# Performance work log

Measured on AMD Instinct MI355X. Metric: run time of the kernel, lower is better.

Reference implementation:

```python
import jax, jax.numpy as jnp
import numpy as np

IN_C = 256
CC = 256
K_HP = 3  # highpass_kernel
ENC_K = 3  # encoder_kernel, dilation 1 -> padding 1


def _conv2d(x, w, b, pad):
    # x: [n, ci, h, w], w: [co, ci, kh, kw] (OIHW), b: [co]
    y = jax.lax.conv_general_dilated(
        x, w, window_strides=(1, 1), padding=((pad, pad), (pad, pad)),
        dimension_numbers=("NCHW", "OIHW", "NCHW"))
    return y + b[None, :, None, None]


def _kernel_normalizer(mask, k, hamming_flat):
    # mask: [n, k*k, h, w] (mask_channel = 1, scale_factor = 1 -> pixel_shuffle is identity)
    n, kc, h, w = mask.shape
    m = jax.nn.softmax(mask, axis=1)              # softmax over the k*k kernel taps
    m = m * hamming_flat[None, :, None, None]     # per-tap hamming window (row-major kxk)
    m = m / jnp.sum(m, axis=1, keepdims=True)     # renormalize to sum 1 per pixel
    return m


def _carafe(x, mask, k):
    # Content-aware reassembly, scale=1, group=1.
    # out[n,c,h,w] = sum_{i,j} mask[n, i*k+j, h, w] * x[n, c, h+i-k//2, w+j-k//2]
    pad = k // 2
    n, c, h, w = x.shape
    xp = jnp.pad(x, ((0, 0), (0, 0), (pad, pad), (pad, pad)))
    out = jnp.zeros_like(x)
    for i in range(k):
        for j in range(k):
            out = out + mask[:, i * k + j][:, None] * xp[:, :, i:i + h, j:j + w]
    return out


def setup_inputs() -> dict:
    key = jax.random.key(0)
    ks = jax.random.split(key, 6)
    n, h, w = 4, 128, 128
    s = 0.02
    x = jax.random.normal(ks[0], (n, IN_C, h, w), jnp.float32)
    w_comp = jax.random.normal(ks[1], (CC, IN_C, 1, 1), jnp.float32) * s
    b_comp = jnp.zeros((CC,), jnp.float32)
    w_hp = jax.random.normal(ks[2], (K_HP * K_HP, CC, ENC_K, ENC_K), jnp.float32) * s
    b_hp = jnp.zeros((K_HP * K_HP,), jnp.float32)
    w_res = jax.random.normal(ks[3], (CC, CC, ENC_K, ENC_K), jnp.float32) * s
    b_res = jnp.zeros((CC,), jnp.float32)
    w_mul = jax.random.normal(ks[4], (CC, CC, ENC_K, ENC_K), jnp.float32) * s
    b_mul = jnp.zeros((CC,), jnp.float32)
    ham = np.outer(np.hamming(K_HP), np.hamming(K_HP)).astype(np.float32).reshape(-1)
    hamming_hp = jnp.asarray(ham)
    return {"x": x, "w_comp": w_comp, "b_comp": b_comp, "w_hp": w_hp, "b_hp": b_hp,
            "w_res": w_res, "b_res": b_res, "w_mul": w_mul, "b_mul": b_mul,
            "hamming_hp": hamming_hp}


def reference(x, w_comp, b_comp, w_hp, b_hp, w_res, b_res, w_mul, b_mul, hamming_hp):
    compressed = _conv2d(x, w_comp, b_comp, 0)
    # high-pass branch: dynamic-kernel generation + CARAFE reassembly
    filt = _conv2d(compressed, w_hp, b_hp, (ENC_K - 1) // 2)
    filt = _kernel_normalizer(filt, K_HP, hamming_hp)
    feat_hp = x - _carafe(x, filt, K_HP)
    # additive residual branch
    feat_add = x + _conv2d(compressed, w_res, b_res, (ENC_K - 1) // 2)
    # multiplicative gating branch
    feat_mul = x * _conv2d(compressed, w_mul, b_mul, (ENC_K - 1) // 2)
    return (feat_hp, feat_add, feat_mul)
```

## Files before the change

### kernel.cpp

```cpp
#include <hip/hip_runtime.h>
#include <hip/hip_bf16.h>

#define NIMG 4
#define C    256
#define H    128
#define W    128
#define HW   (H*W)
#define CHW  (C*HW)
#define TOT  (NIMG*CHW)

typedef short bf16x8 __attribute__((ext_vector_type(8)));
typedef unsigned short ushort8 __attribute__((ext_vector_type(8)));
typedef float f32x16 __attribute__((ext_vector_type(16)));
typedef unsigned short u16;

__device__ inline u16 f2bf(float f) {
    __hip_bfloat16 h = __float2bfloat16(f);
    return __builtin_bit_cast(u16, h);
}

__device__ __forceinline__ int swzB(int byte) {
    return byte ^ (((byte >> 7) & 1) << 4) ^ (((byte >> 8) & 3) << 5);
}

__global__ __launch_bounds__(256)
void prep_w_kernel(const float* __restrict__ w_hp, const float* __restrict__ w_res,
                   const float* __restrict__ w_mul, const float* __restrict__ w_comp,
                   u16* __restrict__ wcat, u16* __restrict__ wbf)
{
    int i = blockIdx.x * 256 + threadIdx.x;
    const int NW = 576 * 2304;
    if (i < NW) {
        int co = i / 2304, r = i - co * 2304;
        int tap = r >> 8, ci = r & 255;
        float v = 0.f;
        if (co < 9)        v = w_hp[co * 2304 + ci * 9 + tap];
        else if (co < 265) v = w_res[(co - 9) * 2304 + ci * 9 + tap];
        else if (co < 521) v = w_mul[(co - 265) * 2304 + ci * 9 + tap];
        wcat[i] = f2bf(v);
    } else if (i < NW + 65536) {
        int j = i - NW;
        wbf[j] = f2bf(w_comp[j]);
    }
}

__global__ __launch_bounds__(256)
void conv1x1_mfma_kernel(const float* __restrict__ x, const u16* __restrict__ wbf,
                         const float* __restrict__ b, u16* __restrict__ comp)
{
    __shared__ u16 As[64 * 40];
    __shared__ u16 Bs[256 * 40];

    const int pt  = blockIdx.x;
    const int n   = pt >> 6;
    const int hw0 = (pt & 63) * 256;
    const int co0 = blockIdx.y * 64;

    const int tid  = threadIdx.x;
    const int wv   = tid >> 6;
    const int lane = tid & 63;
    const int l31  = lane & 31;
    const int lh   = lane >> 5;

    f32x16 acc[2][2];
    #pragma unroll
    for (int cf = 0; cf < 2; ++cf)
        #pragma unroll
        for (int p = 0; p < 2; ++p)
            #pragma unroll
            for (int e = 0; e < 16; ++e) acc[cf][p][e] = 0.f;

    for (int c0 = 0; c0 < 256; c0 += 32) {
        #pragma unroll
        for (int r = 0; r < 2; ++r) {
            int l  = tid + 256*r;
            int co = l >> 3, cq = l & 7;
            ushort4 v = *(const ushort4*)(wbf + (co0+co)*256 + c0 + cq*4);
            *(ushort4*)(As + co*40 + cq*4) = v;
        }
        #pragma unroll
        for (int r = 0; r < 2; ++r) {
            int l = tid + 256*r;
            int q = l & 7, g = l >> 3;
            const float* src = x + (long)n*CHW + (long)(c0 + q*4)*HW + hw0 + g*4;
            float4 v0 = *(const float4*)(src);
            float4 v1 = *(const float4*)(src + HW);
            float4 v2 = *(const float4*)(src + 2*HW);
            float4 v3 = *(const float4*)(src + 3*HW);
            u16* dst = Bs + (g*4)*40 + q*4;
            *(ushort4*)(dst)       = make_ushort4(f2bf(v0.x), f2bf(v1.x), f2bf(v2.x), f2bf(v3.x));
            *(ushort4*)(dst + 40)  = make_ushort4(f2bf(v0.y), f2bf(v1.y), f2bf(v2.y), f2bf(v3.y));
            *(ushort4*)(dst + 80)  = make_ushort4(f2bf(v0.z), f2bf(v1.z), f2bf(v2.z), f2bf(v3.z));
            *(ushort4*)(dst + 120) = make_ushort4(f2bf(v0.w), f2bf(v1.w), f2bf(v2.w), f2bf(v3.w));
        }
        __syncthreads();
        #pragma unroll
        for (int kk = 0; kk < 2; ++kk) {
            bf16x8 a0 = *(const bf16x8*)(As + (l31     )*40 + kk*16 + lh*8);
            bf16x8 a1 = *(const bf16x8*)(As + (l31 + 32)*40 + kk*16 + lh*8);
            #pragma unroll
            for (int p = 0; p < 2; ++p) {
                bf16x8 bb = *(const bf16x8*)(Bs + (wv*64 + p*32 + l31)*40 + kk*16 + lh*8);
                acc[0][p] = __builtin_amdgcn_mfma_f32_32x32x16_bf16(a0, bb, acc[0][p], 0, 0, 0);
                acc[1][p] = __builtin_amdgcn_mfma_f32_32x32x16_bf16(a1, bb, acc[1][p], 0, 0, 0);
            }
        }
        __syncthreads();
    }

    #pragma unroll
    for (int cf = 0; cf < 2; ++cf) {
        #pragma unroll
        for (int p = 0; p < 2; ++p) {
            int pos = hw0 + wv*64 + p*32 + l31;
            #pragma unroll
            for (int reg = 0; reg < 16; ++reg) {
                int row = (reg & 3) + 8*(reg >> 2) + 4*lh;
                int co  = co0 + cf*32 + row;
                comp[(long)n*CHW + (long)co*HW + pos] = f2bf(acc[cf][p][reg] + b[co]);
            }
        }
    }
}

__global__ __launch_bounds__(256, 3)
void conv3x3_mfma_kernel(const u16* __restrict__ comp, const u16* __restrict__ wcat,
                         const float* __restrict__ xin,
                         const float* __restrict__ b_hp, const float* __restrict__ b_res,
                         const float* __restrict__ b_mul,
                         float* __restrict__ out, float* __restrict__ filt_raw)
{
    __shared__ u16 As[64 * 152];
    __shared__ u16 Bs[4 * 132 * 16];

    const int id  = blockIdx.x + 256 * blockIdx.y;
    const int xcd = id & 7;
    const int rr_ = id >> 3;
    const int ct  = rr_ % 9;
    const int pt  = (xcd << 5) + rr_ / 9;

    const int n   = pt >> 6;
    const int y0  = (pt & 63) * 2;
    const int co0 = ct * 64;

    const int tid  = threadIdx.x;
    const int wv   = tid >> 6;
    const int lane = tid & 63;
    const int l31  = lane & 31;
    const int lh   = lane >> 5;
    const int row  = wv & 1;
    const int ch   = wv >> 1;

    for (int i = tid; i < 4*132*16/2; i += 256) ((int*)Bs)[i] = 0;

    f32x16 acc[2][2];
    #pragma unroll
    for (int cf = 0; cf < 2; ++cf)
        #pragma unroll
        for (int p = 0; p < 2; ++p)
            #pragma unroll
            for (int e = 0; e < 16; ++e) acc[cf][p][e] = 0.f;

    const u16* wbase = wcat + (long)co0 * 2304;

    const u16* asrc[5]; u16* adst[5]; bool avld[5];
    #pragma unroll
    for (int r = 0; r < 5; ++r) {
        int l = tid + 256*r;
        avld[r] = (l < 1152);
        int ll = avld[r] ? l : 0;
        int co = ll / 18, s = ll - co*18;
        asrc[r] = wbase + co*2304 + (s >> 1)*256 + (s & 1)*8;
        adst[r] = As + co*152 + s*8;
    }

    const int bh  = lh;
    const int bcg = l31;
    const int byy = y0 - 1 + wv;
    const bool bv = (byy >= 0 && byy < H);
    const u16* bsrc = comp + ((long)n*C + bh*8)*HW + (bv ? byy : 0)*W + bcg*4;

    __syncthreads();

    ushort8 pa[5];
    #pragma unroll
    for (int r = 0; r < 5; ++r)
        if (avld[r]) pa[r] = *(const ushort8*)(asrc[r]);
    ushort4 pb[8];
    if (bv) {
        #pragma unroll
        for (int j = 0; j < 8; ++j) pb[j] = *(const ushort4*)(bsrc + (long)j*HW);
    }

    for (int c = 0; c < 16; ++c) {
        #pragma unroll
        for (int r = 0; r < 5; ++r)
            if (avld[r]) *(ushort8*)(adst[r]) = pa[r];
        if (bv) {
            #pragma unroll
            for (int cw = 0; cw < 4; ++cw) {
                ushort8 v;
                #pragma unroll
                for (int j = 0; j < 8; ++j) v[j] = ((const u16*)&pb[j])[cw];
                int byteoff = ((wv*132 + bcg*4 + 1 + cw) << 5) + (bh << 4);
                *(ushort8*)((char*)Bs + swzB(byteoff)) = v;
            }
        }
        __syncthreads();
        if (c < 15) {
            const int c0n = (c + 1) * 16;
            #pragma unroll
            for (int r = 0; r < 5; ++r)
                if (avld[r]) pa[r] = *(const ushort8*)(asrc[r] + c0n);
            if (bv) {
                const u16* s = bsrc + (long)c0n*HW;
                #pragma unroll
                for (int j = 0; j < 8; ++j) pb[j] = *(const ushort4*)(s + (long)j*HW);
            }
        }
        #pragma unroll
        for (int tap = 0; tap < 9; ++tap) {
            const int kh = tap / 3, kw = tap - kh*3;
            bf16x8 a0 = *(const bf16x8*)((const char*)As + l31*304      + tap*32 + lh*16);
            bf16x8 a1 = *(const bf16x8*)((const char*)As + (l31+32)*304 + tap*32 + lh*16);
            #pragma unroll
            for (int p = 0; p < 2; ++p) {
                int byteoff = (((row + kh)*132 + ch*64 + p*32 + l31 + kw) << 5) + (lh << 4);
                bf16x8 bb = *(const bf16x8*)((const char*)Bs + swzB(byteoff));
                acc[0][p] = __builtin_amdgcn_mfma_f32_32x32x16_bf16(a0, bb, acc[0][p], 0, 0, 0);
                acc[1][p] = __builtin_amdgcn_mfma_f32_32x32x16_bf16(a1, bb, acc[1][p], 0, 0, 0);
            }
        }
        __syncthreads();
    }

    const int yrow = y0 + row;
    #pragma unroll
    for (int cf = 0; cf < 2; ++cf) {
        #pragma unroll
        for (int p = 0; p < 2; ++p) {
            int xx = ch*64 + p*32 + l31;
            #pragma unroll
            for (int reg = 0; reg < 16; ++reg) {
                int rw = (reg & 3) + 8*(reg >> 2) + 4*lh;
                int co = co0 + cf*32 + rw;
                float v = acc[cf][p][reg];
                if (co < 9) {
                    filt_raw[((long)n*9 + co)*HW + yrow*W + xx] = v + b_hp[co];
                } else if (co < 265) {
                    int cc = co - 9;
                    long idx = (long)n*CHW + (long)cc*HW + yrow*W + xx;
                    out[(long)TOT + idx] = xin[idx] + v + b_res[cc];
                } else if (co < 521) {
                    int cc = co - 265;
                    long idx = (long)n*CHW + (long)cc*HW + yrow*W + xx;
                    out[2L*TOT + idx] = xin[idx] * (v + b_mul[cc]);
                }
            }
        }
    }
}

__global__ __launch_bounds__(256)
void carafe_hp_kernel(const float* __restrict__ x, const float* __restrict__ filt_raw,
                      const float* __restrict__ ham, float* __restrict__ out)
{
    const int id = blockIdx.x;
    const int pt = ((id & 7) << 6) + (id >> 3);
    const int n  = pt >> 7;
    const int y  = pt & 127;
    const int pg = threadIdx.x & 31;
    const int cs = threadIdx.x >> 5;
    const int x0 = pg * 4;

    float4 wt[9];
    {
        const float* fr = filt_raw + (long)n*9*HW + y*W + x0;
        #pragma unroll
        for (int t = 0; t < 9; ++t) wt[t] = *(const float4*)(fr + t*HW);
        float4 mx = wt[0];
        #pragma unroll
        for (int t = 1; t < 9; ++t) {
            mx.x = fmaxf(mx.x, wt[t].x); mx.y = fmaxf(mx.y, wt[t].y);
            mx.z = fmaxf(mx.z, wt[t].z); mx.w = fmaxf(mx.w, wt[t].w);
        }
        float4 s = make_float4(0,0,0,0);
        #pragma unroll
        for (int t = 0; t < 9; ++t) {
            float hm = ham[t];
            wt[t].x = expf(wt[t].x - mx.x) * hm; s.x += wt[t].x;
            wt[t].y = expf(wt[t].y - mx.y) * hm; s.y += wt[t].y;
            wt[t].z = expf(wt[t].z - mx.z) * hm; s.z += wt[t].z;
            wt[t].w = expf(wt[t].w - mx.w) * hm; s.w += wt[t].w;
        }
        float4 inv = make_float4(1.f/s.x, 1.f/s.y, 1.f/s.z, 1.f/s.w);
        #pragma unroll
        for (int t = 0; t < 9; ++t) {
            wt[t].x *= inv.x; wt[t].y *= inv.y; wt[t].z *= inv.z; wt[t].w *= inv.w;
        }
    }

    const float* xb = x   + (long)n*CHW + (long)y*W + x0;
    float*       ob = out + (long)n*CHW + (long)y*W + x0;

    for (int i = 0; i < 32; ++i) {
        int c = cs*32 + i;
        const float* xc = xb + (long)c*HW;
        float rr[3][6];
        #pragma unroll
        for (int dh = 0; dh < 3; ++dh) {
            int yy = y - 1 + dh;
            if (yy >= 0 && yy < H) {
                const float* p = xc + (dh-1)*W;
                float4 v = *(const float4*)p;
                rr[dh][0] = (x0 > 0)     ? p[-1] : 0.f;
                rr[dh][1] = v.x; rr[dh][2] = v.y; rr[dh][3] = v.z; rr[dh][4] = v.w;
                rr[dh][5] = (x0 + 4 < W) ? p[4]  : 0.f;
            } else {
                #pragma unroll
                for (int j = 0; j < 6; ++j) rr[dh][j] = 0.f;
            }
        }
        float4 a = make_float4(0,0,0,0);
        #pragma unroll
        for (int dh = 0; dh < 3; ++dh)
            #pragma unroll
            for (int kw = 0; kw < 3; ++kw) {
                float4 wv = wt[dh*3+kw];
                a.x += wv.x * rr[dh][kw];
                a.y += wv.y * rr[dh][kw+1];
                a.z += wv.z * rr[dh][kw+2];
                a.w += wv.w * rr[dh][kw+3];
            }
        float4 o;
        o.x = rr[1][1] - a.x; o.y = rr[1][2] - a.y;
        o.z = rr[1][3] - a.z; o.w = rr[1][4] - a.w;
        *(float4*)(ob + (long)c*HW) = o;
    }
}

extern "C" void kernel_launch(void* const* d_in, const int* in_sizes, int n_in,
                              void* d_out, int out_size, void* d_ws, size_t ws_size,
                              hipStream_t stream)
{
    const float* x      = (const float*)d_in[0];
    const float* w_comp = (const float*)d_in[1];
    const float* b_comp = (const float*)d_in[2];
    const float* w_hp   = (const float*)d_in[3];
    const float* b_hp   = (const float*)d_in[4];
    const float* w_res  = (const float*)d_in[5];
    const float* b_res  = (const float*)d_in[6];
    const float* w_mul  = (const float*)d_in[7];
    const float* b_mul  = (const float*)d_in[8];
    const float* ham    = (const float*)d_in[9];
    float* out = (float*)d_out;

    u16*   comp = (u16*)d_ws;
    float* filt = (float*)((char*)d_ws + (size_t)TOT*2);
    u16*   wcat = (u16*)((char*)d_ws + (size_t)TOT*2 + 2359296);
    u16*   wbf  = (u16*)((char*)d_ws + (size_t)TOT*2 + 2359296 + 2654208);

    const int NW = 576*2304;
    prep_w_kernel<<<(NW + 65536 + 255)/256, 256, 0, stream>>>(w_hp, w_res, w_mul, w_comp, wcat, wbf);
    conv1x1_mfma_kernel<<<dim3(256, 4), 256, 0, stream>>>(x, wbf, b_comp, comp);
    conv3x3_mfma_kernel<<<dim3(NIMG*H/2, 9), 256, 0, stream>>>(
        comp, wcat, x, b_hp, b_res, b_mul, out, filt);
    carafe_hp_kernel<<<NIMG*H, 256, 0, stream>>>(x, filt, ham, out);
}
```

Measured before the change: 315.1 us.

## Enlarge conv3x3 tile to four output rows per block to reuse weights

The fused 3x3 conv kernel now computes four output rows per block instead of two. Each wave handles two rows, which doubles the accumulators and lets every A-fragment load feed twice as many MFMAs. The shared halo buffer grows from 4 to 6 rows and the grid halves to 1152 blocks, cutting redundant weight loads and halo overhead. The cost is higher register pressure (occupancy hint lowered from 3 to 2) and fewer blocks to spread across the CUs.

```diff
diff --git a/kernel.cpp b/kernel.cpp
--- a/kernel.cpp
+++ b/kernel.cpp
@@ -123,7 +123,7 @@
     }
 }
 
-__global__ __launch_bounds__(256, 3)
+__global__ __launch_bounds__(256, 2)
 void conv3x3_mfma_kernel(const u16* __restrict__ comp, const u16* __restrict__ wcat,
                          const float* __restrict__ xin,
                          const float* __restrict__ b_hp, const float* __restrict__ b_res,
@@ -131,16 +131,16 @@
                          float* __restrict__ out, float* __restrict__ filt_raw)
 {
     __shared__ u16 As[64 * 152];
-    __shared__ u16 Bs[4 * 132 * 16];
-
-    const int id  = blockIdx.x + 256 * blockIdx.y;
+    __shared__ u16 Bs[6 * 132 * 16];
+
+    const int id  = blockIdx.x;
     const int xcd = id & 7;
     const int rr_ = id >> 3;
     const int ct  = rr_ % 9;
-    const int pt  = (xcd << 5) + rr_ / 9;
-
-    const int n   = pt >> 6;
-    const int y0  = (pt & 63) * 2;
+    const int pt  = (xcd << 4) + rr_ / 9;
+
+    const int n   = pt >> 5;
+    const int y0  = (pt & 31) * 4;
     const int co0 = ct * 64;
 
     const int tid  = threadIdx.x;
@@ -148,18 +148,20 @@
     const int lane = tid & 63;
     const int l31  = lane & 31;
     const int lh   = lane >> 5;
-    const int row  = wv & 1;
-    const int ch   = wv >> 1;
-
-    for (int i = tid; i < 4*132*16/2; i += 256) ((int*)Bs)[i] = 0;
-
-    f32x16 acc[2][2];
+    const int ch   = wv & 1;
+    const int rv   = wv >> 1;
+
+    for (int i = tid; i < 6*132*16/2; i += 256) ((int*)Bs)[i] = 0;
+
+    f32x16 acc[2][2][2];
     #pragma unroll
     for (int cf = 0; cf < 2; ++cf)
         #pragma unroll
-        for (int p = 0; p < 2; ++p)
-            #pragma unroll
-            for (int e = 0; e < 16; ++e) acc[cf][p][e] = 0.f;
+        for (int r2 = 0; r2 < 2; ++r2)
+            #pragma unroll
+            for (int p = 0; p < 2; ++p)
+                #pragma unroll
+                for (int e = 0; e < 16; ++e) acc[cf][r2][p][e] = 0.f;
 
     const u16* wbase = wcat + (long)co0 * 2304;
 
@@ -174,11 +176,20 @@
         adst[r] = As + co*152 + s*8;
     }
 
-    const int bh  = lh;
-    const int bcg = l31;
-    const int byy = y0 - 1 + wv;
-    const bool bv = (byy >= 0 && byy < H);
-    const u16* bsrc = comp + ((long)n*C + bh*8)*HW + (bv ? byy : 0)*W + bcg*4;
+    const int pr1  = tid >> 6;
+    const int bh1  = (tid >> 5) & 1;
+    const int cg1  = tid & 31;
+    const int y1   = y0 - 1 + pr1;
+    const bool bv1 = (y1 >= 0 && y1 < H);
+    const u16* bsrc1 = comp + ((long)n*C + bh1*8)*HW + (bv1 ? y1 : 0)*W + cg1*4;
+
+    const bool has2 = (tid < 128);
+    const int pr2  = 4 + (tid >> 6);
+    const int bh2  = (tid >> 5) & 1;
+    const int cg2  = tid & 31;
+    const int y2   = y0 - 1 + pr2;
+    const bool bv2 = has2 && (y2 >= 0 && y2 < H);
+    const u16* bsrc2 = comp + ((long)n*C + bh2*8)*HW + (bv2 ? y2 : 0)*W + cg2*4;
 
     __syncthreads();
 
@@ -186,23 +197,37 @@
     #pragma unroll
     for (int r = 0; r < 5; ++r)
         if (avld[r]) pa[r] = *(const ushort8*)(asrc[r]);
-    ushort4 pb[8];
-    if (bv) {
-        #pragma unroll
-        for (int j = 0; j < 8; ++j) pb[j] = *(const ushort4*)(bsrc + (long)j*HW);
+    ushort4 pb1[8], pb2[8];
+    if (bv1) {
+        #pragma unroll
+        for (int j = 0; j < 8; ++j) pb1[j] = *(const ushort4*)(bsrc1 + (long)j*HW);
+    }
+    if (bv2) {
+        #pragma unroll
+        for (int j = 0; j < 8; ++j) pb2[j] = *(const ushort4*)(bsrc2 + (long)j*HW);
     }
 
     for (int c = 0; c < 16; ++c) {
         #pragma unroll
         for (int r = 0; r < 5; ++r)
             if (avld[r]) *(ushort8*)(adst[r]) = pa[r];
-        if (bv) {
+        if (bv1) {
             #pragma unroll
             for (int cw = 0; cw < 4; ++cw) {
                 ushort8 v;
                 #pragma unroll
-                for (int j = 0; j < 8; ++j) v[j] = ((const u16*)&pb[j])[cw];
-                int byteoff = ((wv*132 + bcg*4 + 1 + cw) << 5) + (bh << 4);
+                for (int j = 0; j < 8; ++j) v[j] = ((const u16*)&pb1[j])[cw];
+                int byteoff = ((pr1*132 + cg1*4 + 1 + cw) << 5) + (bh1 << 4);
+                *(ushort8*)((char*)Bs + swzB(byteoff)) = v;
+            }
+        }
+        if (bv2) {
+            #pragma unroll
+            for (int cw = 0; cw < 4; ++cw) {
+                ushort8 v;
+                #pragma unroll
+                for (int j = 0; j < 8; ++j) v[j] = ((const u16*)&pb2[j])[cw];
+                int byteoff = ((pr2*132 + cg2*4 + 1 + cw) << 5) + (bh2 << 4);
                 *(ushort8*)((char*)Bs + swzB(byteoff)) = v;
             }
         }
@@ -212,10 +237,15 @@
             #pragma unroll
             for (int r = 0; r < 5; ++r)
                 if (avld[r]) pa[r] = *(const ushort8*)(asrc[r] + c0n);
-            if (bv) {
-                const u16* s = bsrc + (long)c0n*HW;
-                #pragma unroll
-                for (int j = 0; j < 8; ++j) pb[j] = *(const ushort4*)(s + (long)j*HW);
+            if (bv1) {
+                const u16* s = bsrc1 + (long)c0n*HW;
+                #pragma unroll
+                for (int j = 0; j < 8; ++j) pb1[j] = *(const ushort4*)(s + (long)j*HW);
+            }
+            if (bv2) {
+                const u16* s = bsrc2 + (long)c0n*HW;
+                #pragma unroll
+                for (int j = 0; j < 8; ++j) pb2[j] = *(const ushort4*)(s + (long)j*HW);
             }
         }
         #pragma unroll
@@ -224,37 +254,44 @@
             bf16x8 a0 = *(const bf16x8*)((const char*)As + l31*304      + tap*32 + lh*16);
             bf16x8 a1 = *(const bf16x8*)((const char*)As + (l31+32)*304 + tap*32 + lh*16);
             #pragma unroll
+            for (int r2 = 0; r2 < 2; ++r2) {
+                const int slot = 2*rv + r2 + kh;
+                #pragma unroll
+                for (int p = 0; p < 2; ++p) {
+                    int byteoff = ((slot*132 + ch*64 + p*32 + l31 + kw) << 5) + (lh << 4);
+                    bf16x8 bb = *(const bf16x8*)((const char*)Bs + swzB(byteoff));
+                    acc[0][r2][p] = __builtin_amdgcn_mfma_f32_32x32x16_bf16(a0, bb, acc[0][r2][p], 0, 0, 0);
+                    acc[1][r2][p] = __builtin_amdgcn_mfma_f32_32x32x16_bf16(a1, bb, acc[1][r2][p], 0, 0, 0);
+                }
+            }
+        }
+        __syncthreads();
+    }
+
+    #pragma unroll
+    for (int cf = 0; cf < 2; ++cf) {
+        #pragma unroll
+        for (int r2 = 0; r2 < 2; ++r2) {
+            const int yrow = y0 + 2*rv + r2;
+            #pragma unroll
             for (int p = 0; p < 2; ++p) {
-                int byteoff = (((row + kh)*132 + ch*64 + p*32 + l31 + kw) << 5) + (lh << 4);
-                bf16x8 bb = *(const bf16x8*)((const char*)Bs + swzB(byteoff));
-                acc[0][p] = __builtin_amdgcn_mfma_f32_32x32x16_bf16(a0, bb, acc[0][p], 0, 0, 0);
-                acc[1][p] = __builtin_amdgcn_mfma_f32_32x32x16_bf16(a1, bb, acc[1][p], 0, 0, 0);
-            }
-        }
-        __syncthreads();
-    }
-
-    const int yrow = y0 + row;
-    #pragma unroll
-    for (int cf = 0; cf < 2; ++cf) {
-        #pragma unroll
-        for (int p = 0; p < 2; ++p) {
-            int xx = ch*64 + p*32 + l31;
-            #pragma unroll
-            for (int reg = 0; reg < 16; ++reg) {
-                int rw = (reg & 3) + 8*(reg >> 2) + 4*lh;
-                int co = co0 + cf*32 + rw;
-                float v = acc[cf][p][reg];
-                if (co < 9) {
-                    filt_raw[((long)n*9 + co)*HW + yrow*W + xx] = v + b_hp[co];
-                } else if (co < 265) {
-                    int cc = co - 9;
-                    long idx = (long)n*CHW + (long)cc*HW + yrow*W + xx;
-                    out[(long)TOT + idx] = xin[idx] + v + b_res[cc];
-                } else if (co < 521) {
-                    int cc = co - 265;
-                    long idx = (long)n*CHW + (long)cc*HW + yrow*W + xx;
-                    out[2L*TOT + idx] = xin[idx] * (v + b_mul[cc]);
+                int xx = ch*64 + p*32 + l31;
+                #pragma unroll
+                for (int reg = 0; reg < 16; ++reg) {
+                    int rw = (reg & 3) + 8*(reg >> 2) + 4*lh;
+                    int co = co0 + cf*32 + rw;
+                    float v = acc[cf][r2][p][reg];
+                    if (co < 9) {
+                        filt_raw[((long)n*9 + co)*HW + yrow*W + xx] = v + b_hp[co];
+                    } else if (co < 265) {
+                        int cc = co - 9;
+                        long idx = (long)n*CHW + (long)cc*HW + yrow*W + xx;
+                        out[(long)TOT + idx] = xin[idx] + v + b_res[cc];
+                    } else if (co < 521) {
+                        int cc = co - 265;
+                        long idx = (long)n*CHW + (long)cc*HW + yrow*W + xx;
+                        out[2L*TOT + idx] = xin[idx] * (v + b_mul[cc]);
+                    }
                 }
             }
         }
@@ -363,7 +400,7 @@
     const int NW = 576*2304;
     prep_w_kernel<<<(NW + 65536 + 255)/256, 256, 0, stream>>>(w_hp, w_res, w_mul, w_comp, wcat, wbf);
     conv1x1_mfma_kernel<<<dim3(256, 4), 256, 0, stream>>>(x, wbf, b_comp, comp);
-    conv3x3_mfma_kernel<<<dim3(NIMG*H/2, 9), 256, 0, stream>>>(
+    conv3x3_mfma_kernel<<<1152, 256, 0, stream>>>(
         comp, wcat, x, b_hp, b_res, b_mul, out, filt);
     carafe_hp_kernel<<<NIMG*H, 256, 0, stream>>>(x, filt, ham, out);
 }
```

Measured after the change: 388.5 us (median of 3 runs). 1.23x slower.

## Pre-swizzle conv weights into MFMA fragment order and load A directly to registers

Applied to the files above, without the earlier changes.

The weight prep kernel now writes the concatenated 3x3 weights in the exact per-lane MFMA A-fragment order, indexed by channel tile, tap and channel chunk. The 3x3 conv kernel drops its shared-memory A tile and loads A fragments from global memory straight into registers, prefetching three taps ahead in a small rotating buffer. This removes the LDS writes and reads for weights and shrinks shared memory per block. In exchange, more global and L2 loads land inside the inner MFMA loop, and their latency may be exposed.

```diff
diff --git a/kernel.cpp b/kernel.cpp
--- a/kernel.cpp
+++ b/kernel.cpp
@@ -31,12 +31,20 @@
     int i = blockIdx.x * 256 + threadIdx.x;
     const int NW = 576 * 2304;
     if (i < NW) {
-        int co = i / 2304, r = i - co * 2304;
-        int tap = r >> 8, ci = r & 255;
+        int e   = i & 7;
+        int l31 = (i >> 3) & 31;
+        int lhh = (i >> 8) & 1;
+        int coh = (i >> 9) & 1;
+        int cq  = (i >> 10) & 15;
+        int t9  = i >> 14;
+        int ct  = t9 / 9;
+        int tap = t9 - ct * 9;
+        int gco = ct*64 + coh*32 + l31;
+        int ci  = cq*16 + lhh*8 + e;
         float v = 0.f;
-        if (co < 9)        v = w_hp[co * 2304 + ci * 9 + tap];
-        else if (co < 265) v = w_res[(co - 9) * 2304 + ci * 9 + tap];
-        else if (co < 521) v = w_mul[(co - 265) * 2304 + ci * 9 + tap];
+        if (gco < 9)        v = w_hp[gco * 2304 + ci * 9 + tap];
+        else if (gco < 265) v = w_res[(gco - 9) * 2304 + ci * 9 + tap];
+        else if (gco < 521) v = w_mul[(gco - 265) * 2304 + ci * 9 + tap];
         wcat[i] = f2bf(v);
     } else if (i < NW + 65536) {
         int j = i - NW;
@@ -124,13 +132,12 @@
 }
 
 __global__ __launch_bounds__(256, 3)
-void conv3x3_mfma_kernel(const u16* __restrict__ comp, const u16* __restrict__ wcat,
+void conv3x3_mfma_kernel(const u16* __restrict__ wcat, const u16* __restrict__ comp,
                          const float* __restrict__ xin,
                          const float* __restrict__ b_hp, const float* __restrict__ b_res,
                          const float* __restrict__ b_mul,
                          float* __restrict__ out, float* __restrict__ filt_raw)
 {
-    __shared__ u16 As[64 * 152];
     __shared__ u16 Bs[4 * 132 * 16];
 
     const int id  = blockIdx.x + 256 * blockIdx.y;
@@ -161,68 +168,55 @@
             #pragma unroll
             for (int e = 0; e < 16; ++e) acc[cf][p][e] = 0.f;
 
-    const u16* wbase = wcat + (long)co0 * 2304;
-
-    const u16* asrc[5]; u16* adst[5]; bool avld[5];
-    #pragma unroll
-    for (int r = 0; r < 5; ++r) {
-        int l = tid + 256*r;
-        avld[r] = (l < 1152);
-        int ll = avld[r] ? l : 0;
-        int co = ll / 18, s = ll - co*18;
-        asrc[r] = wbase + co*2304 + (s >> 1)*256 + (s & 1)*8;
-        adst[r] = As + co*152 + s*8;
-    }
-
-    const int bh  = lh;
-    const int bcg = l31;
+    const u16* wt0 = wcat + (long)ct*147456 + lh*256 + l31*8;
+
     const int byy = y0 - 1 + wv;
     const bool bv = (byy >= 0 && byy < H);
-    const u16* bsrc = comp + ((long)n*C + bh*8)*HW + (bv ? byy : 0)*W + bcg*4;
+    const u16* bsrc = comp + ((long)n*C + lh*8)*HW + (bv ? byy : 0)*W + l31*4;
 
     __syncthreads();
 
-    ushort8 pa[5];
-    #pragma unroll
-    for (int r = 0; r < 5; ++r)
-        if (avld[r]) pa[r] = *(const ushort8*)(asrc[r]);
     ushort4 pb[8];
     if (bv) {
         #pragma unroll
         for (int j = 0; j < 8; ++j) pb[j] = *(const ushort4*)(bsrc + (long)j*HW);
     }
+    bf16x8 af0[3], af1[3];
+    #pragma unroll
+    for (int t = 0; t < 3; ++t) {
+        af0[t] = *(const bf16x8*)(wt0 + t*16384);
+        af1[t] = *(const bf16x8*)(wt0 + t*16384 + 512);
+    }
 
     for (int c = 0; c < 16; ++c) {
-        #pragma unroll
-        for (int r = 0; r < 5; ++r)
-            if (avld[r]) *(ushort8*)(adst[r]) = pa[r];
         if (bv) {
             #pragma unroll
             for (int cw = 0; cw < 4; ++cw) {
                 ushort8 v;
                 #pragma unroll
                 for (int j = 0; j < 8; ++j) v[j] = ((const u16*)&pb[j])[cw];
-                int byteoff = ((wv*132 + bcg*4 + 1 + cw) << 5) + (bh << 4);
+                int byteoff = ((wv*132 + l31*4 + 1 + cw) << 5) + (lh << 4);
                 *(ushort8*)((char*)Bs + swzB(byteoff)) = v;
             }
         }
         __syncthreads();
-        if (c < 15) {
-            const int c0n = (c + 1) * 16;
-            #pragma unroll
-            for (int r = 0; r < 5; ++r)
-                if (avld[r]) pa[r] = *(const ushort8*)(asrc[r] + c0n);
-            if (bv) {
-                const u16* s = bsrc + (long)c0n*HW;
-                #pragma unroll
-                for (int j = 0; j < 8; ++j) pb[j] = *(const ushort4*)(s + (long)j*HW);
-            }
+        if (c < 15 && bv) {
+            const u16* s = bsrc + (long)(c + 1)*16*HW;
+            #pragma unroll
+            for (int j = 0; j < 8; ++j) pb[j] = *(const ushort4*)(s + (long)j*HW);
         }
         #pragma unroll
         for (int tap = 0; tap < 9; ++tap) {
             const int kh = tap / 3, kw = tap - kh*3;
-            bf16x8 a0 = *(const bf16x8*)((const char*)As + l31*304      + tap*32 + lh*16);
-            bf16x8 a1 = *(const bf16x8*)((const char*)As + (l31+32)*304 + tap*32 + lh*16);
+            const int r_ = tap % 3;
+            bf16x8 a0 = af0[r_], a1 = af1[r_];
+            if (tap < 6) {
+                af0[r_] = *(const bf16x8*)(wt0 + (tap+3)*16384 + c*1024);
+                af1[r_] = *(const bf16x8*)(wt0 + (tap+3)*16384 + c*1024 + 512);
+            } else if (c < 15) {
+                af0[r_] = *(const bf16x8*)(wt0 + (tap-6)*16384 + (c+1)*1024);
+                af1[r_] = *(const bf16x8*)(wt0 + (tap-6)*16384 + (c+1)*1024 + 512);
+            }
             #pragma unroll
             for (int p = 0; p < 2; ++p) {
                 int byteoff = (((row + kh)*132 + ch*64 + p*32 + l31 + kw) << 5) + (lh << 4);
@@ -364,6 +358,6 @@
     prep_w_kernel<<<(NW + 65536 + 255)/256, 256, 0, stream>>>(w_hp, w_res, w_mul, w_comp, wcat, wbf);
     conv1x1_mfma_kernel<<<dim3(256, 4), 256, 0, stream>>>(x, wbf, b_comp, comp);
     conv3x3_mfma_kernel<<<dim3(NIMG*H/2, 9), 256, 0, stream>>>(
-        comp, wcat, x, b_hp, b_res, b_mul, out, filt);
+        wcat, comp, x, b_hp, b_res, b_mul, out, filt);
     carafe_hp_kernel<<<NIMG*H, 256, 0, stream>>>(x, filt, ham, out);
 }
```

Measured after the change: 320.2 us. No clear change (+1.6%).
